# Kernel optimization log

Hardware: AMD Instinct MI355X
Metric: run time of the kernel (lower is better)

The kernel has to match this reference:

```python
import jax, jax.numpy as jnp
import numpy as np

B, L, D, H, NE, M = 4, 1024, 768, 12, 42, 8
P = NE * (NE - 1)
OFFSET = 1  # BERT [CLS] offset, matching self.offset = 1
EPS = 1e-5


def setup_inputs() -> dict:
    key = jax.random.key(0)
    k1, k2, k3, k4 = jax.random.split(key, 4)
    sequence_output = jax.random.normal(k1, (B, L, D), dtype=jnp.float32)
    # post-softmax attention probs are nonnegative
    attention = jax.random.uniform(k2, (B, H, L, L), dtype=jnp.float32)
    mention_pos = jax.random.randint(k3, (B, NE, M), 0, L - 2)
    mask = (jax.random.uniform(k4, (B, NE, M)) < 0.5).astype(jnp.float32)
    mention_mask = mask.at[:, :, 0].set(1.0)  # every entity has >= 1 mention
    # hts: all ordered entity pairs (h != t), same for every doc
    ii, jj = jnp.meshgrid(jnp.arange(NE), jnp.arange(NE), indexing='ij')
    pairs = jnp.stack([ii.ravel(), jj.ravel()], axis=-1)
    pairs = pairs[np.asarray(ii.ravel() != jj.ravel())]  # [P, 2]
    hts = jnp.broadcast_to(pairs[None], (B, P, 2)).astype(jnp.int64)
    return dict(sequence_output=sequence_output, attention=attention,
                mention_mask=mention_mask,
                mention_pos=mention_pos.astype(jnp.int64), hts=hts)


def reference(sequence_output, attention, mention_mask, mention_pos, hts):
    idx = mention_pos + OFFSET  # [B, NE, M], all < L by construction

    # --- get_entity_embed: gather mention-start token embeds, masked logsumexp over mentions ---
    m_emb = jax.vmap(lambda so, i: so[i])(sequence_output, idx)  # [B, NE, M, D]
    neg = jnp.finfo(m_emb.dtype).min
    entity_embed = jax.nn.logsumexp(
        jnp.where(mention_mask[..., None] > 0, m_emb, neg), axis=2)  # [B, NE, D]

    # --- get_hrt: gather attention rows at mention starts, masked mean over mentions ---
    m_att = jax.vmap(lambda att, i: att[:, i])(attention, idx)  # [B, H, NE, M, L]
    mm = mention_mask[:, None, :, :, None]                      # [B, 1, NE, M, 1]
    entity_att = (m_att * mm).sum(3) / mm.sum(3)                # [B, H, NE, L]

    # --- get_channel_map: all-pairs head*tail attention, mean over heads, normalize, contract ---
    ht_att = jnp.einsum('bhil,bhjl->bijl', entity_att, entity_att) / H  # [B, NE, NE, L]
    ht_att = ht_att / (ht_att.sum(-1, keepdims=True) + EPS)
    feature_map = jnp.einsum('bijl,bld->bijd', ht_att, sequence_output)  # [B, NE, NE, D]

    # --- get_ht: gather per-pair features ---
    h_t = jax.vmap(lambda fm, ht: fm[ht[:, 0], ht[:, 1]])(feature_map, hts)  # [B, P, D]
    return entity_embed, h_t.reshape(B * P, D)
```

## Files before the change

kernel.cpp:

```cpp
#include <hip/hip_runtime.h>
#include <hip/hip_bf16.h>
#include <math.h>

constexpr int Bn  = 4;
constexpr int Ln  = 1024;
constexpr int Dn  = 768;
constexpr int Hn  = 12;
constexpr int NEn = 42;
constexpr int Mn  = 8;
constexpr int Pn  = NEn * (NEn - 1);
constexpr int OFFn = 1;
constexpr float EPSn = 1e-5f;
constexpr int CL = 32;
constexpr int CHUNKS = Ln / CL;
constexpr int HALFP = Pn / 2;
constexpr int LDSW = 40;

constexpr int SOT_BLKS = (Ln / 32) * (Dn / 32) * Bn;
constexpr int EA_BLKS  = Bn * Hn * NEn;

typedef __attribute__((ext_vector_type(8))) short bf16x8;
typedef __attribute__((ext_vector_type(4))) float f32x4;

__device__ inline unsigned short f2bf(float v) {
    unsigned u = __float_as_uint(v);
    u += 0x7fffu + ((u >> 16) & 1u);
    return (unsigned short)(u >> 16);
}

__global__ __launch_bounds__(256) void k_entity_embed(
    const float* __restrict__ so, const float* __restrict__ mask,
    const int* __restrict__ mpos, float* __restrict__ out)
{
    const int be = blockIdx.x;
    const int b = be / NEn, e = be % NEn;
    __shared__ int   s_idx[Mn];
    __shared__ float s_msk[Mn];
    if (threadIdx.x < Mn) {
        const int m = threadIdx.x;
        s_idx[m] = mpos[(b * NEn + e) * Mn + m] + OFFn;
        s_msk[m] = mask[(b * NEn + e) * Mn + m];
    }
    __syncthreads();
    for (int d = threadIdx.x; d < Dn; d += 256) {
        float v[Mn];
        float mx = -3.4e38f;
        #pragma unroll
        for (int m = 0; m < Mn; ++m) {
            const float val = so[((size_t)b * Ln + s_idx[m]) * Dn + d];
            v[m] = (s_msk[m] > 0.f) ? val : -3.4e38f;
            mx = fmaxf(mx, v[m]);
        }
        float s = 0.f;
        #pragma unroll
        for (int m = 0; m < Mn; ++m)
            s += (v[m] > -3.0e38f) ? __expf(v[m] - mx) : 0.f;
        out[((size_t)b * NEn + e) * Dn + d] = mx + __logf(s);
    }
}

__global__ __launch_bounds__(256) void k_prep(
    const float* __restrict__ so, const float* __restrict__ att,
    const float* __restrict__ mask, const int* __restrict__ mpos,
    unsigned short* __restrict__ soT, unsigned short* __restrict__ ea2)
{
    const int bx = blockIdx.x;
    if (bx < SOT_BLKS) {
        __shared__ unsigned short tile[32][33];
        const int rem = bx % ((Ln / 32) * (Dn / 32));
        const int b   = bx / ((Ln / 32) * (Dn / 32));
        const int l0  = (rem % (Ln / 32)) * 32;
        const int d0  = (rem / (Ln / 32)) * 32;
        const int cx = threadIdx.x & 31;
        const int ry = threadIdx.x >> 5;
        for (int r = ry; r < 32; r += 8)
            tile[r][cx] = f2bf(so[((size_t)b * Ln + l0 + r) * Dn + d0 + cx]);
        __syncthreads();
        for (int r = ry; r < 32; r += 8)
            soT[((size_t)b * Dn + d0 + r) * Ln + l0 + cx] = tile[cx][r];
    } else {
        const int id = bx - SOT_BLKS;
        const int e = id % NEn;
        const int bh = id / NEn;
        const int h = bh % Hn;
        const int b = bh / Hn;
        __shared__ int   s_idx[Mn];
        __shared__ float s_w[Mn];
        __shared__ float s_inv;
        if (threadIdx.x == 0) {
            float sum = 0.f;
            for (int m = 0; m < Mn; ++m) {
                s_idx[m] = mpos[(b * NEn + e) * Mn + m] + OFFn;
                const float w = mask[(b * NEn + e) * Mn + m];
                s_w[m] = w; sum += w;
            }
            s_inv = 1.f / sum;
        }
        __syncthreads();
        const int l = threadIdx.x * 4;
        float4 acc = {0.f, 0.f, 0.f, 0.f};
        #pragma unroll
        for (int m = 0; m < Mn; ++m) {
            if (s_w[m] > 0.f) {
                const float4 v = *(const float4*)&att[(((size_t)b * Hn + h) * Ln + s_idx[m]) * Ln + l];
                acc.x += v.x; acc.y += v.y; acc.z += v.z; acc.w += v.w;
            }
        }
        const unsigned u0 = (unsigned)f2bf(acc.x * s_inv) | ((unsigned)f2bf(acc.y * s_inv) << 16);
        const unsigned u1 = (unsigned)f2bf(acc.z * s_inv) | ((unsigned)f2bf(acc.w * s_inv) << 16);
        uint2 uu; uu.x = u0; uu.y = u1;
        *(uint2*)&ea2[((size_t)id) * Ln + l] = uu;
    }
}

__global__ __launch_bounds__(256) void k_pairs(
    const unsigned short* __restrict__ ea2, unsigned short* __restrict__ xb,
    float* __restrict__ Spart)
{
    __shared__ unsigned sm[Hn * NEn * 17];
    const int c    = blockIdx.x;
    const int half = blockIdx.y;
    const int b    = blockIdx.z;
    const int t    = threadIdx.x;

    const unsigned* eg = (const unsigned*)ea2 + ((size_t)b * Hn * NEn) * (Ln / 2) + c * (CL / 2);
    for (int id = t; id < Hn * NEn * 16; id += 256) {
        const int r = id >> 4, u = id & 15;
        sm[r * 17 + u] = eg[(size_t)r * (Ln / 2) + u];
    }
    __syncthreads();

    const int l2 = t & 15;
    const int pm = t >> 4;
    const int rend = (half + 1) * HALFP;
    unsigned* xbu = (unsigned*)xb;
    for (int rk = half * HALFP + pm; rk < rend; rk += 16) {
        const int i  = rk / (NEn - 1);
        const int jj = rk % (NEn - 1);
        const int j  = jj + (jj >= i ? 1 : 0);
        float a0 = 0.f, a1 = 0.f;
        #pragma unroll
        for (int h = 0; h < Hn; ++h) {
            const unsigned ui = sm[(h * NEn + i) * 17 + l2];
            const unsigned uj = sm[(h * NEn + j) * 17 + l2];
            const float xi0 = __uint_as_float(ui << 16);
            const float xi1 = __uint_as_float(ui & 0xffff0000u);
            const float xj0 = __uint_as_float(uj << 16);
            const float xj1 = __uint_as_float(uj & 0xffff0000u);
            a0 = fmaf(xi0, xj0, a0);
            a1 = fmaf(xi1, xj1, a1);
        }
        xbu[((size_t)b * Pn + rk) * (Ln / 2) + c * (CL / 2) + l2] =
            (unsigned)f2bf(a0) | ((unsigned)f2bf(a1) << 16);
        float part = a0 + a1;
        part += __shfl_down(part, 8, 16);
        part += __shfl_down(part, 4, 16);
        part += __shfl_down(part, 2, 16);
        part += __shfl_down(part, 1, 16);
        if (l2 == 0)
            Spart[((size_t)b * CHUNKS + c) * Pn + rk] = part;
    }
}

__global__ __launch_bounds__(256) void k_gemm_mfma(
    const unsigned short* __restrict__ xb, const unsigned short* __restrict__ soT,
    const float* __restrict__ Spart, float* __restrict__ out2)
{
    __shared__ __align__(16) unsigned short As[2][128 * LDSW];
    __shared__ __align__(16) unsigned short Bs[2][128 * LDSW];
    __shared__ float s_scale[128];

    const int row0 = blockIdx.x * 128;
    const int col0 = blockIdx.y * 128;
    const int b    = blockIdx.z;
    const int t    = threadIdx.x;
    const int lane = t & 63;
    const int wave = t >> 6;
    const int wm = wave & 1, wn = wave >> 1;

    if (t < 128) {
        const int r = min(row0 + t, Pn - 1);
        float s = 0.f;
        #pragma unroll
        for (int cix = 0; cix < CHUNKS; ++cix)
            s += Spart[((size_t)b * CHUNKS + cix) * Pn + r];
        s_scale[t] = 1.0f / (s + (float)Hn * EPSn);
    }

    f32x4 acc[4][4];
    #pragma unroll
    for (int i2 = 0; i2 < 4; ++i2)
        #pragma unroll
        for (int j2 = 0; j2 < 4; ++j2)
            acc[i2][j2] = (f32x4){0.f, 0.f, 0.f, 0.f};

    const int sr = t >> 2;
    const int sc = (t & 3) * 8;
    const int arow0 = min(row0 + sr,      Pn - 1);
    const int arow1 = min(row0 + sr + 64, Pn - 1);
    const size_t abase0 = ((size_t)b * Pn + arow0) * Ln + sc;
    const size_t abase1 = ((size_t)b * Pn + arow1) * Ln + sc;
    const size_t bbase0 = ((size_t)b * Dn + col0 + sr) * Ln + sc;
    const size_t bbase1 = ((size_t)b * Dn + col0 + sr + 64) * Ln + sc;

    const int fr = lane & 15;
    const int fo = (lane >> 4) * 8;

    bf16x8 a0 = *(const bf16x8*)(xb  + abase0);
    bf16x8 a1 = *(const bf16x8*)(xb  + abase1);
    bf16x8 b0 = *(const bf16x8*)(soT + bbase0);
    bf16x8 b1 = *(const bf16x8*)(soT + bbase1);
    *(bf16x8*)&As[0][sr * LDSW + sc]        = a0;
    *(bf16x8*)&As[0][(sr + 64) * LDSW + sc] = a1;
    *(bf16x8*)&Bs[0][sr * LDSW + sc]        = b0;
    *(bf16x8*)&Bs[0][(sr + 64) * LDSW + sc] = b1;
    __syncthreads();

    for (int k0 = 0; k0 < 32; ++k0) {
        const int cur = k0 & 1;
        if (k0 < 31) {
            const int kn = (k0 + 1) * 32;
            a0 = *(const bf16x8*)(xb  + abase0 + kn);
            a1 = *(const bf16x8*)(xb  + abase1 + kn);
            b0 = *(const bf16x8*)(soT + bbase0 + kn);
            b1 = *(const bf16x8*)(soT + bbase1 + kn);
        }

        bf16x8 af[4], bfr[4];
        #pragma unroll
        for (int mt = 0; mt < 4; ++mt)
            af[mt] = *(const bf16x8*)&As[cur][(wm * 64 + mt * 16 + fr) * LDSW + fo];
        #pragma unroll
        for (int nt = 0; nt < 4; ++nt)
            bfr[nt] = *(const bf16x8*)&Bs[cur][(wn * 64 + nt * 16 + fr) * LDSW + fo];
        #pragma unroll
        for (int mt = 0; mt < 4; ++mt)
            #pragma unroll
            for (int nt = 0; nt < 4; ++nt)
                acc[mt][nt] = __builtin_amdgcn_mfma_f32_16x16x32_bf16(
                    af[mt], bfr[nt], acc[mt][nt], 0, 0, 0);

        if (k0 < 31) {
            const int nxt = cur ^ 1;
            *(bf16x8*)&As[nxt][sr * LDSW + sc]        = a0;
            *(bf16x8*)&As[nxt][(sr + 64) * LDSW + sc] = a1;
            *(bf16x8*)&Bs[nxt][sr * LDSW + sc]        = b0;
            *(bf16x8*)&Bs[nxt][(sr + 64) * LDSW + sc] = b1;
            __syncthreads();
        }
    }

    const int ccol  = lane & 15;
    const int crow4 = (lane >> 4) * 4;
    #pragma unroll
    for (int mt = 0; mt < 4; ++mt) {
        #pragma unroll
        for (int rg = 0; rg < 4; ++rg) {
            const int ml = wm * 64 + mt * 16 + crow4 + rg;
            const int r  = row0 + ml;
            if (r < Pn) {
                const float sc2 = s_scale[ml];
                float* dst = out2 + ((size_t)b * Pn + r) * Dn + col0 + wn * 64 + ccol;
                #pragma unroll
                for (int nt = 0; nt < 4; ++nt)
                    dst[nt * 16] = acc[mt][nt][rg] * sc2;
            }
        }
    }
}

extern "C" void kernel_launch(void* const* d_in, const int* in_sizes, int n_in,
                              void* d_out, int out_size, void* d_ws, size_t ws_size,
                              hipStream_t stream)
{
    const float* so   = (const float*)d_in[0];
    const float* att  = (const float*)d_in[1];
    const float* mask = (const float*)d_in[2];
    const int*   mpos = (const int*)d_in[3];
    float* out = (float*)d_out;
    float* out_ee = out;
    float* out_ht = out + (size_t)Bn * NEn * Dn;

    char* w = (char*)d_ws;
    unsigned short* ea2 = (unsigned short*)w; w += (size_t)Bn * Hn * NEn * Ln * 2;
    unsigned short* xb  = (unsigned short*)w; w += (size_t)Bn * Pn * Ln * 2;
    unsigned short* soT = (unsigned short*)w; w += (size_t)Bn * Dn * Ln * 2;
    float* Spart = (float*)w;

    hipLaunchKernelGGL(k_prep, dim3(SOT_BLKS + EA_BLKS), dim3(256), 0, stream,
                       so, att, mask, mpos, soT, ea2);
    hipLaunchKernelGGL(k_pairs, dim3(CHUNKS, 2, Bn), dim3(256), 0, stream,
                       ea2, xb, Spart);
    hipLaunchKernelGGL(k_gemm_mfma, dim3((Pn + 127) / 128, Dn / 128, Bn), dim3(256), 0, stream,
                       xb, soT, Spart, out_ht);
    hipLaunchKernelGGL(k_entity_embed, dim3(Bn * NEn), dim3(256), 0, stream,
                       so, mask, mpos, out_ee);
}
```

Before: 317.4 us.

## Load GEMM tiles directly into LDS with XOR swizzle and XCD-aware block remap

The MFMA GEMM now stages A and B tiles through global_load_lds direct-to-LDS loads instead of register round trips. The padded LDS row layout is replaced by an unpadded 32-wide layout with an XOR swizzle on the 16-byte column groups to avoid bank conflicts. The 3D grid is flattened into a 1D grid whose block index is permuted across the 8 XCDs for better L2 locality. This frees registers and VALU/LDS-store instructions, but relies on the lane-to-LDS mapping of direct loads matching the swizzle, and still needs a barrier every k-step.

Result: no change. 315.3 us (-0.7%).

```diff
diff --git a/kernel.cpp b/kernel.cpp
--- a/kernel.cpp
+++ b/kernel.cpp
@@ -14,7 +14,6 @@
 constexpr int CL = 32;
 constexpr int CHUNKS = Ln / CL;
 constexpr int HALFP = Pn / 2;
-constexpr int LDSW = 40;
 
 constexpr int SOT_BLKS = (Ln / 32) * (Dn / 32) * Bn;
 constexpr int EA_BLKS  = Bn * Hn * NEn;
@@ -26,6 +25,12 @@
     unsigned u = __float_as_uint(v);
     u += 0x7fffu + ((u >> 16) & 1u);
     return (unsigned short)(u >> 16);
+}
+
+__device__ inline void gld16(const unsigned short* g, unsigned short* l) {
+    typedef __attribute__((address_space(3))) unsigned lds_u32;
+    typedef const __attribute__((address_space(1))) unsigned glb_u32;
+    __builtin_amdgcn_global_load_lds((glb_u32*)g, (lds_u32*)(uintptr_t)l, 16, 0, 0);
 }
 
 __global__ __launch_bounds__(256) void k_entity_embed(
@@ -166,13 +171,20 @@
     const unsigned short* __restrict__ xb, const unsigned short* __restrict__ soT,
     const float* __restrict__ Spart, float* __restrict__ out2)
 {
-    __shared__ __align__(16) unsigned short As[2][128 * LDSW];
-    __shared__ __align__(16) unsigned short Bs[2][128 * LDSW];
+    __shared__ __align__(16) unsigned short As[2][128 * 32];
+    __shared__ __align__(16) unsigned short Bs[2][128 * 32];
     __shared__ float s_scale[128];
 
-    const int row0 = blockIdx.x * 128;
-    const int col0 = blockIdx.y * 128;
-    const int b    = blockIdx.z;
+    constexpr int nbx = (Pn + 127) / 128;
+    constexpr int nby = Dn / 128;
+    constexpr int nwg = nbx * nby * Bn;
+    int bid = (int)blockIdx.x;
+    bid = (bid & 7) * (nwg >> 3) + (bid >> 3);
+    const int b    = bid / (nbx * nby);
+    const int rem  = bid % (nbx * nby);
+    const int row0 = (rem % nbx) * 128;
+    const int col0 = (rem / nbx) * 128;
+
     const int t    = threadIdx.x;
     const int lane = t & 63;
     const int wave = t >> 6;
@@ -194,45 +206,46 @@
         for (int j2 = 0; j2 < 4; ++j2)
             acc[i2][j2] = (f32x4){0.f, 0.f, 0.f, 0.f};
 
-    const int sr = t >> 2;
-    const int sc = (t & 3) * 8;
-    const int arow0 = min(row0 + sr,      Pn - 1);
-    const int arow1 = min(row0 + sr + 64, Pn - 1);
-    const size_t abase0 = ((size_t)b * Pn + arow0) * Ln + sc;
-    const size_t abase1 = ((size_t)b * Pn + arow1) * Ln + sc;
-    const size_t bbase0 = ((size_t)b * Dn + col0 + sr) * Ln + sc;
-    const size_t bbase1 = ((size_t)b * Dn + col0 + sr + 64) * Ln + sc;
-
-    const int fr = lane & 15;
-    const int fo = (lane >> 4) * 8;
-
-    bf16x8 a0 = *(const bf16x8*)(xb  + abase0);
-    bf16x8 a1 = *(const bf16x8*)(xb  + abase1);
-    bf16x8 b0 = *(const bf16x8*)(soT + bbase0);
-    bf16x8 b1 = *(const bf16x8*)(soT + bbase1);
-    *(bf16x8*)&As[0][sr * LDSW + sc]        = a0;
-    *(bf16x8*)&As[0][(sr + 64) * LDSW + sc] = a1;
-    *(bf16x8*)&Bs[0][sr * LDSW + sc]        = b0;
-    *(bf16x8*)&Bs[0][(sr + 64) * LDSW + sc] = b1;
+    const int rqa = t >> 2;
+    const int rqb = rqa + 64;
+    const int cq  = t & 3;
+    const int sca = (cq ^ ((rqa >> 1) & 3)) * 8;
+    const int scb = (cq ^ ((rqb >> 1) & 3)) * 8;
+    const unsigned short* gA0 = xb  + ((size_t)b * Pn + min(row0 + rqa, Pn - 1)) * Ln + sca;
+    const unsigned short* gA1 = xb  + ((size_t)b * Pn + min(row0 + rqb, Pn - 1)) * Ln + scb;
+    const unsigned short* gB0 = soT + ((size_t)b * Dn + col0 + rqa) * Ln + sca;
+    const unsigned short* gB1 = soT + ((size_t)b * Dn + col0 + rqb) * Ln + scb;
+    const int ldsOff0 = (wave << 6) * 8;
+    const int ldsOff1 = ldsOff0 + 256 * 8;
+
+    const int fr   = lane & 15;
+    const int koq  = lane >> 4;
+    const int coff = (koq ^ ((fr >> 1) & 3)) * 8;
+
+    gld16(gA0, &As[0][ldsOff0]);
+    gld16(gA1, &As[0][ldsOff1]);
+    gld16(gB0, &Bs[0][ldsOff0]);
+    gld16(gB1, &Bs[0][ldsOff1]);
     __syncthreads();
 
     for (int k0 = 0; k0 < 32; ++k0) {
         const int cur = k0 & 1;
         if (k0 < 31) {
-            const int kn = (k0 + 1) * 32;
-            a0 = *(const bf16x8*)(xb  + abase0 + kn);
-            a1 = *(const bf16x8*)(xb  + abase1 + kn);
-            b0 = *(const bf16x8*)(soT + bbase0 + kn);
-            b1 = *(const bf16x8*)(soT + bbase1 + kn);
+            const int koff = (k0 + 1) * 32;
+            const int nxt = cur ^ 1;
+            gld16(gA0 + koff, &As[nxt][ldsOff0]);
+            gld16(gA1 + koff, &As[nxt][ldsOff1]);
+            gld16(gB0 + koff, &Bs[nxt][ldsOff0]);
+            gld16(gB1 + koff, &Bs[nxt][ldsOff1]);
         }
 
         bf16x8 af[4], bfr[4];
         #pragma unroll
         for (int mt = 0; mt < 4; ++mt)
-            af[mt] = *(const bf16x8*)&As[cur][(wm * 64 + mt * 16 + fr) * LDSW + fo];
+            af[mt] = *(const bf16x8*)&As[cur][(wm * 64 + mt * 16 + fr) * 32 + coff];
         #pragma unroll
         for (int nt = 0; nt < 4; ++nt)
-            bfr[nt] = *(const bf16x8*)&Bs[cur][(wn * 64 + nt * 16 + fr) * LDSW + fo];
+            bfr[nt] = *(const bf16x8*)&Bs[cur][(wn * 64 + nt * 16 + fr) * 32 + coff];
         #pragma unroll
         for (int mt = 0; mt < 4; ++mt)
             #pragma unroll
@@ -240,14 +253,7 @@
                 acc[mt][nt] = __builtin_amdgcn_mfma_f32_16x16x32_bf16(
                     af[mt], bfr[nt], acc[mt][nt], 0, 0, 0);
 
-        if (k0 < 31) {
-            const int nxt = cur ^ 1;
-            *(bf16x8*)&As[nxt][sr * LDSW + sc]        = a0;
-            *(bf16x8*)&As[nxt][(sr + 64) * LDSW + sc] = a1;
-            *(bf16x8*)&Bs[nxt][sr * LDSW + sc]        = b0;
-            *(bf16x8*)&Bs[nxt][(sr + 64) * LDSW + sc] = b1;
-            __syncthreads();
-        }
+        __syncthreads();
     }
 
     const int ccol  = lane & 15;
@@ -291,7 +297,7 @@
                        so, att, mask, mpos, soT, ea2);
     hipLaunchKernelGGL(k_pairs, dim3(CHUNKS, 2, Bn), dim3(256), 0, stream,
                        ea2, xb, Spart);
-    hipLaunchKernelGGL(k_gemm_mfma, dim3((Pn + 127) / 128, Dn / 128, Bn), dim3(256), 0, stream,
+    hipLaunchKernelGGL(k_gemm_mfma, dim3((Pn + 127) / 128 * (Dn / 128) * Bn), dim3(256), 0, stream,
                        xb, soT, Spart, out_ht);
     hipLaunchKernelGGL(k_entity_embed, dim3(Bn * NEn), dim3(256), 0, stream,
                        so, mask, mpos, out_ee);
```
